# Optimization experiments

Hardware: AMD Instinct MI355X
Metric: run time of the kernel (lower is better)

## Reference

```python
import jax, jax.numpy as jnp
import numpy as np

DIM = 64
HEADS = 4
N_NODES = 50000
N_EDGES = 800000
NEG_SLOPE = 0.2


def setup_inputs() -> dict:
    key = jax.random.key(0)
    k1, k2, k3, k4, k5 = jax.random.split(key, 5)
    meta_x = jax.random.normal(k1, (N_NODES, DIM), dtype=jnp.float32)
    meta_edge_index = jax.random.randint(k2, (2, N_EDGES), 0, N_NODES, dtype=jnp.int64)
    # GATConv params: shared source/dest Linear (no bias), per-head attention vecs, output bias.
    glorot = float(np.sqrt(2.0 / (DIM + HEADS * DIM)))
    W = jax.random.normal(k3, (DIM, HEADS * DIM), dtype=jnp.float32) * glorot  # x @ W
    att_src = jax.random.normal(k4, (1, HEADS, DIM), dtype=jnp.float32) * glorot
    att_dst = jax.random.normal(k5, (1, HEADS, DIM), dtype=jnp.float32) * glorot
    bias = jnp.zeros((DIM,), dtype=jnp.float32)
    return {"meta_x": meta_x, "meta_edge_index": meta_edge_index,
            "W": W, "att_src": att_src, "att_dst": att_dst, "bias": bias}


def reference(meta_x, meta_edge_index, W, att_src, att_dst, bias):
    N = meta_x.shape[0]
    # PyG GATConv default: add self-loops
    loops = jnp.arange(N, dtype=meta_edge_index.dtype)
    edge = jnp.concatenate([meta_edge_index, jnp.stack([loops, loops])], axis=1)
    src, dst = edge[0], edge[1]

    x = (meta_x @ W).reshape(N, HEADS, DIM)            # [N, H, C]
    a_src = jnp.sum(x * att_src, axis=-1)              # [N, H]
    a_dst = jnp.sum(x * att_dst, axis=-1)              # [N, H]

    logits = a_src[src] + a_dst[dst]                   # [E, H]
    logits = jax.nn.leaky_relu(logits, NEG_SLOPE)

    # segment softmax over edges grouped by destination node
    seg_max = jax.ops.segment_max(logits, dst, num_segments=N)   # [N, H]
    ex = jnp.exp(logits - seg_max[dst])
    seg_sum = jax.ops.segment_sum(ex, dst, num_segments=N)
    alpha = ex / (seg_sum[dst] + 1e-16)                # [E, H]

    msg = x[src] * alpha[:, :, None]                   # [E, H, C]
    out = jax.ops.segment_sum(msg, dst, num_segments=N)  # [N, H, C]
    # concat=False -> mean over heads, then bias
    return out.mean(axis=1) + bias
```

## Files before the change

kernel.cpp:

```cpp
#include <hip/hip_runtime.h>
#include <hip/hip_bf16.h>
#include <math.h>

#define MAXDEG 64

__device__ __forceinline__ float lrelu(float v) { return v > 0.0f ? v : 0.2f * v; }

__global__ void prep_kernel(int4* __restrict__ cnt4, int n4, int N,
                            const float* __restrict__ W, const float* __restrict__ att_src,
                            const float* __restrict__ att_dst, float* __restrict__ wsrc,
                            float* __restrict__ wdst) {
  int idx = blockIdx.x * 256 + threadIdx.x;
  for (int i = idx; i < n4; i += gridDim.x * 256) {
    int base = i * 4;
    int4 v;
    v.x = (base < N) ? 1 : 0;
    v.y = (base + 1 < N) ? 1 : 0;
    v.z = (base + 2 < N) ? 1 : 0;
    v.w = (base + 3 < N) ? 1 : 0;
    cnt4[i] = v;
  }
  if (blockIdx.x == 0) {
    int t = threadIdx.x;
    int h = t >> 6, k = t & 63;
    const float* wrow = W + (size_t)k * 256 + h * 64;
    const float* as = att_src + h * 64;
    const float* ad = att_dst + h * 64;
    float ss = 0.f, sd = 0.f;
#pragma unroll
    for (int c = 0; c < 64; ++c) {
      float w = wrow[c];
      ss = fmaf(w, as[c], ss);
      sd = fmaf(w, ad[c], sd);
    }
    wsrc[k * 4 + h] = ss;
    wdst[k * 4 + h] = sd;
  }
}

__global__ void nh_kernel(const float* __restrict__ x, const float4* __restrict__ wsrc4,
                          const float4* __restrict__ wdst4, float4* __restrict__ asrc4,
                          float4* __restrict__ adst4, __hip_bfloat16* __restrict__ xh,
                          const int* __restrict__ ei, int* __restrict__ counts,
                          int E, int N, int nbh) {
  if (blockIdx.x < nbh) {
    int slice = blockIdx.x & 7;
    int bid = blockIdx.x >> 3;
    int nb = nbh >> 3;
    int chunk = (N + 7) >> 3;
    int lo = slice * chunk;
    int hi = lo + chunk; if (hi > N) hi = N;
    int E4 = E >> 2;
    const int4* d4p = (const int4*)(ei + E);
    int stride = nb * 256;
    for (int i = bid * 256 + threadIdx.x; i < E4; i += stride) {
      int4 d = d4p[i];
      if (d.x >= lo && d.x < hi) atomicAdd(&counts[d.x], 1);
      if (d.y >= lo && d.y < hi) atomicAdd(&counts[d.y], 1);
      if (d.z >= lo && d.z < hi) atomicAdd(&counts[d.z], 1);
      if (d.w >= lo && d.w < hi) atomicAdd(&counts[d.w], 1);
    }
    return;
  }
  int lane = threadIdx.x & 63;
  int n = (blockIdx.x - nbh) * 4 + (threadIdx.x >> 6);
  if (n >= N) return;
  float xv = x[(size_t)n * 64 + lane];
  xh[(size_t)n * 64 + lane] = __float2bfloat16(xv);
  float4 ws = wsrc4[lane], wd = wdst4[lane];
  float s0 = xv * ws.x, s1 = xv * ws.y, s2 = xv * ws.z, s3 = xv * ws.w;
  float d0 = xv * wd.x, d1 = xv * wd.y, d2 = xv * wd.z, d3 = xv * wd.w;
#pragma unroll
  for (int m = 1; m < 64; m <<= 1) {
    s0 += __shfl_xor(s0, m, 64); s1 += __shfl_xor(s1, m, 64);
    s2 += __shfl_xor(s2, m, 64); s3 += __shfl_xor(s3, m, 64);
    d0 += __shfl_xor(d0, m, 64); d1 += __shfl_xor(d1, m, 64);
    d2 += __shfl_xor(d2, m, 64); d3 += __shfl_xor(d3, m, 64);
  }
  if (lane == 0) {
    asrc4[n] = make_float4(s0, s1, s2, s3);
    adst4[n] = make_float4(d0, d1, d2, d3);
  }
}

__global__ void nattn_kernel(const float* __restrict__ x, const float4* __restrict__ wsrc4,
                             const float4* __restrict__ wdst4, float4* __restrict__ asrc4,
                             float4* __restrict__ adst4, __hip_bfloat16* __restrict__ xh,
                             int N) {
  int lane = threadIdx.x & 63;
  int n = blockIdx.x * 4 + (threadIdx.x >> 6);
  if (n >= N) return;
  float xv = x[(size_t)n * 64 + lane];
  xh[(size_t)n * 64 + lane] = __float2bfloat16(xv);
  float4 ws = wsrc4[lane], wd = wdst4[lane];
  float s0 = xv * ws.x, s1 = xv * ws.y, s2 = xv * ws.z, s3 = xv * ws.w;
  float d0 = xv * wd.x, d1 = xv * wd.y, d2 = xv * wd.z, d3 = xv * wd.w;
#pragma unroll
  for (int m = 1; m < 64; m <<= 1) {
    s0 += __shfl_xor(s0, m, 64); s1 += __shfl_xor(s1, m, 64);
    s2 += __shfl_xor(s2, m, 64); s3 += __shfl_xor(s3, m, 64);
    d0 += __shfl_xor(d0, m, 64); d1 += __shfl_xor(d1, m, 64);
    d2 += __shfl_xor(d2, m, 64); d3 += __shfl_xor(d3, m, 64);
  }
  if (lane == 0) {
    asrc4[n] = make_float4(s0, s1, s2, s3);
    adst4[n] = make_float4(d0, d1, d2, d3);
  }
}

__global__ void hist_kernel(const int* __restrict__ ei, int* __restrict__ counts, int E) {
  int e = blockIdx.x * 256 + threadIdx.x;
  if (e >= E) return;
  atomicAdd(&counts[ei[(size_t)E + e]], 1);
}

__global__ void scatter_kernel(const int* __restrict__ ei, int* __restrict__ cursor,
                               int* __restrict__ src_sorted, int E, int N) {
  int e = blockIdx.x * 256 + threadIdx.x;
  int ET = E + N;
  if (e >= ET) return;
  int src, dst;
  if (e < E) {
    src = ei[e];
    dst = ei[(size_t)E + e];
  } else {
    src = dst = e - E;
  }
  int pos = atomicAdd(&cursor[dst], 1);
  src_sorted[pos] = src;
}

__global__ void scatter8_kernel(const int* __restrict__ ei, int* __restrict__ cursor,
                                int* __restrict__ srt, int E, int N) {
  int slice = blockIdx.x & 7;
  int bid = blockIdx.x >> 3;
  int nb = gridDim.x >> 3;
  int chunk = (N + 7) >> 3;
  int lo = slice * chunk;
  int hi = lo + chunk; if (hi > N) hi = N;
  int E4 = E >> 2;
  const int4* s4p = (const int4*)ei;
  const int4* d4p = (const int4*)(ei + E);
  int stride = nb * 256;
  for (int i = bid * 256 + threadIdx.x; i < E4; i += stride) {
    int4 d4 = d4p[i];
    bool bx = (d4.x >= lo && d4.x < hi), by = (d4.y >= lo && d4.y < hi);
    bool bz = (d4.z >= lo && d4.z < hi), bw = (d4.w >= lo && d4.w < hi);
    if (!(bx || by || bz || bw)) continue;
    int4 s4 = s4p[i];
    if (bx) { int p = atomicAdd(&cursor[d4.x], 1); srt[p] = s4.x; }
    if (by) { int p = atomicAdd(&cursor[d4.y], 1); srt[p] = s4.y; }
    if (bz) { int p = atomicAdd(&cursor[d4.z], 1); srt[p] = s4.z; }
    if (bw) { int p = atomicAdd(&cursor[d4.w], 1); srt[p] = s4.w; }
  }
  for (int n = lo + bid * 256 + threadIdx.x; n < hi; n += stride) {
    int p = atomicAdd(&cursor[n], 1);
    srt[p] = n;
  }
}

__global__ void scanABC_kernel(const int* __restrict__ cnt, int* __restrict__ row,
                               int* __restrict__ cur, int N, int ntiles) {
  __shared__ int tl[256];
  __shared__ int part[256];
  int b = blockIdx.x, t = threadIdx.x;
  int s = 0;
  if (t < ntiles) {
    const int4* c4 = (const int4*)cnt + t * 64;
    for (int i = 0; i < 64; ++i) {
      int4 v = c4[i];
      s += v.x + v.y + v.z + v.w;
    }
  }
  tl[t] = s;
  __syncthreads();
  for (int d = 1; d < 256; d <<= 1) {
    int u = (t >= d) ? tl[t - d] : 0;
    __syncthreads();
    tl[t] += u;
    __syncthreads();
  }
  int tileoff = (b == 0) ? 0 : tl[b - 1];
  int idx = b * 256 + t;
  int c = (idx < N) ? cnt[idx] : 0;
  part[t] = c;
  __syncthreads();
  for (int d = 1; d < 256; d <<= 1) {
    int u = (t >= d) ? part[t - d] : 0;
    __syncthreads();
    part[t] += u;
    __syncthreads();
  }
  int exc = part[t] - c + tileoff;
  if (idx < N) {
    row[idx] = exc;
    cur[idx] = exc;
    if (idx == N - 1) row[N] = exc + c;
  }
}

__global__ void scanA_kernel(const int* __restrict__ cnt, int* __restrict__ tsum, int N) {
  int b = blockIdx.x, t = threadIdx.x;
  int idx = b * 256 + t;
  int v = (idx < N) ? cnt[idx] : 0;
#pragma unroll
  for (int m = 1; m < 64; m <<= 1) v += __shfl_xor(v, m, 64);
  __shared__ int ws[4];
  if ((t & 63) == 0) ws[t >> 6] = v;
  __syncthreads();
  if (t == 0) tsum[b] = ws[0] + ws[1] + ws[2] + ws[3];
}

__global__ void scanB_kernel(int* __restrict__ tsum, int ntiles) {
  __shared__ int part[256];
  int t = threadIdx.x;
  int carry = 0;
  for (int b0 = 0; b0 < ntiles; b0 += 256) {
    int idx = b0 + t;
    int v = (idx < ntiles) ? tsum[idx] : 0;
    part[t] = v;
    __syncthreads();
    for (int d = 1; d < 256; d <<= 1) {
      int u = (t >= d) ? part[t - d] : 0;
      __syncthreads();
      part[t] += u;
      __syncthreads();
    }
    if (idx < ntiles) tsum[idx] = part[t] - v + carry;
    carry += part[255];
    __syncthreads();
  }
}

__global__ void scanC_kernel(const int* __restrict__ cnt, const int* __restrict__ tsum,
                             int* __restrict__ row, int* __restrict__ cur, int N) {
  __shared__ int part[256];
  int b = blockIdx.x, t = threadIdx.x;
  int idx = b * 256 + t;
  int c = (idx < N) ? cnt[idx] : 0;
  part[t] = c;
  __syncthreads();
  for (int d = 1; d < 256; d <<= 1) {
    int u = (t >= d) ? part[t - d] : 0;
    __syncthreads();
    part[t] += u;
    __syncthreads();
  }
  int exc = part[t] - c + tsum[b];
  if (idx < N) {
    row[idx] = exc;
    cur[idx] = exc;
    if (idx == N - 1) row[N] = exc + c;
  }
}

__global__ __launch_bounds__(256) void agg_kernel(
    const int* __restrict__ srt, const int* __restrict__ row,
    const float4* __restrict__ asrc4, const float4* __restrict__ adst4,
    const __hip_bfloat16* __restrict__ xh, __hip_bfloat16* __restrict__ agg, int N) {
  __shared__ float4 alL[4][MAXDEG];
  __shared__ int slL[4][MAXDEG];
  int t = threadIdx.x, w = t >> 6, lane = t & 63;
  int n = blockIdx.x * 4 + w;
  if (n >= N) return;
  int start = row[n], end = row[n + 1];
  int deg = end - start;
  float4 ad = adst4[n];
  float t0 = 0.f, t1 = 0.f, t2 = 0.f, t3 = 0.f;
  if (deg <= MAXDEG) {
    for (int b = 0; b < deg; b += 64) {
      if (b + lane < deg) {
        int sl = srt[start + b + lane];
        float4 as = asrc4[sl];
        float4 e;
        e.x = __expf(lrelu(as.x + ad.x));
        e.y = __expf(lrelu(as.y + ad.y));
        e.z = __expf(lrelu(as.z + ad.z));
        e.w = __expf(lrelu(as.w + ad.w));
        alL[w][b + lane] = e;
        slL[w][b + lane] = sl;
        t0 += e.x; t1 += e.y; t2 += e.z; t3 += e.w;
      }
    }
  } else {
    for (int b = start; b < end; b += 64) {
      int idx = b + lane;
      if (idx < end) {
        int sl = srt[idx];
        float4 as = asrc4[sl];
        t0 += __expf(lrelu(as.x + ad.x));
        t1 += __expf(lrelu(as.y + ad.y));
        t2 += __expf(lrelu(as.z + ad.z));
        t3 += __expf(lrelu(as.w + ad.w));
      }
    }
  }
#pragma unroll
  for (int m = 1; m < 64; m <<= 1) {
    t0 += __shfl_xor(t0, m, 64);
    t1 += __shfl_xor(t1, m, 64);
    t2 += __shfl_xor(t2, m, 64);
    t3 += __shfl_xor(t3, m, 64);
  }
  float r0 = 0.25f / (t0 + 1e-16f), r1 = 0.25f / (t1 + 1e-16f);
  float r2 = 0.25f / (t2 + 1e-16f), r3 = 0.25f / (t3 + 1e-16f);
  float a0 = 0.f, a1 = 0.f, a2 = 0.f, a3 = 0.f;
  if (deg <= MAXDEG) {
    int j = 0;
    for (; j + 4 <= deg; j += 4) {
      float4 e0 = alL[w][j], e1 = alL[w][j + 1], e2 = alL[w][j + 2], e3 = alL[w][j + 3];
      int q0 = slL[w][j], q1 = slL[w][j + 1], q2 = slL[w][j + 2], q3 = slL[w][j + 3];
      float v0 = __bfloat162float(xh[(size_t)q0 * 64 + lane]);
      float v1 = __bfloat162float(xh[(size_t)q1 * 64 + lane]);
      float v2 = __bfloat162float(xh[(size_t)q2 * 64 + lane]);
      float v3 = __bfloat162float(xh[(size_t)q3 * 64 + lane]);
      a0 = fmaf(e0.x, v0, a0); a1 = fmaf(e0.y, v0, a1);
      a2 = fmaf(e0.z, v0, a2); a3 = fmaf(e0.w, v0, a3);
      a0 = fmaf(e1.x, v1, a0); a1 = fmaf(e1.y, v1, a1);
      a2 = fmaf(e1.z, v1, a2); a3 = fmaf(e1.w, v1, a3);
      a0 = fmaf(e2.x, v2, a0); a1 = fmaf(e2.y, v2, a1);
      a2 = fmaf(e2.z, v2, a2); a3 = fmaf(e2.w, v2, a3);
      a0 = fmaf(e3.x, v3, a0); a1 = fmaf(e3.y, v3, a1);
      a2 = fmaf(e3.z, v3, a2); a3 = fmaf(e3.w, v3, a3);
    }
    for (; j < deg; ++j) {
      float4 e0 = alL[w][j];
      int q0 = slL[w][j];
      float v0 = __bfloat162float(xh[(size_t)q0 * 64 + lane]);
      a0 = fmaf(e0.x, v0, a0); a1 = fmaf(e0.y, v0, a1);
      a2 = fmaf(e0.z, v0, a2); a3 = fmaf(e0.w, v0, a3);
    }
  } else {
    for (int b = start; b < end; b += 64) {
      int cnt = end - b;
      if (cnt > 64) cnt = 64;
      int idx = b + lane;
      int sl = 0;
      float e0 = 0.f, e1 = 0.f, e2 = 0.f, e3 = 0.f;
      if (idx < end) {
        sl = srt[idx];
        float4 as = asrc4[sl];
        e0 = __expf(lrelu(as.x + ad.x));
        e1 = __expf(lrelu(as.y + ad.y));
        e2 = __expf(lrelu(as.z + ad.z));
        e3 = __expf(lrelu(as.w + ad.w));
      }
      for (int j = 0; j < cnt; ++j) {
        int sj = __shfl(sl, j, 64);
        float b0 = __shfl(e0, j, 64), b1 = __shfl(e1, j, 64);
        float b2 = __shfl(e2, j, 64), b3 = __shfl(e3, j, 64);
        float v = __bfloat162float(xh[(size_t)sj * 64 + lane]);
        a0 = fmaf(b0, v, a0); a1 = fmaf(b1, v, a1);
        a2 = fmaf(b2, v, a2); a3 = fmaf(b3, v, a3);
      }
    }
  }
  __hip_bfloat16* ao = agg + (size_t)n * 256;
  ao[lane] = __float2bfloat16(a0 * r0);
  ao[64 + lane] = __float2bfloat16(a1 * r1);
  ao[128 + lane] = __float2bfloat16(a2 * r2);
  ao[192 + lane] = __float2bfloat16(a3 * r3);
}

__global__ __launch_bounds__(256) void proj_kernel(
    const __hip_bfloat16* __restrict__ agg, const float* __restrict__ W,
    const float* __restrict__ bias, float* __restrict__ out, int N) {
  __shared__ float aggL[4][256];
  __shared__ float pL[4][4][64];
  int t = threadIdx.x, w = t >> 6, lane = t & 63;
  float Wreg[64];
#pragma unroll
  for (int k = 0; k < 64; ++k) Wreg[k] = W[(size_t)k * 256 + w * 64 + lane];
  float bv = bias[lane];
  int ngroups = (N + 3) >> 2;
  for (int g = blockIdx.x; g < ngroups; g += gridDim.x) {
    int n0 = g * 4;
    __syncthreads();
    {
      int nn = n0 + w;
      if (nn < N) {
        ushort4 u = ((const ushort4*)(agg + (size_t)nn * 256))[t & 63];
        float4 f;
        f.x = __bfloat162float(*(__hip_bfloat16*)&u.x);
        f.y = __bfloat162float(*(__hip_bfloat16*)&u.y);
        f.z = __bfloat162float(*(__hip_bfloat16*)&u.z);
        f.w = __bfloat162float(*(__hip_bfloat16*)&u.w);
        *(float4*)&aggL[w][(t & 63) * 4] = f;
      } else {
        *(float4*)&aggL[w][(t & 63) * 4] = make_float4(0.f, 0.f, 0.f, 0.f);
      }
    }
    __syncthreads();
    float acc0 = 0.f, acc1 = 0.f, acc2 = 0.f, acc3 = 0.f;
#pragma unroll
    for (int k4 = 0; k4 < 16; ++k4) {
      float4 av0 = *(const float4*)&aggL[0][w * 64 + k4 * 4];
      float4 av1 = *(const float4*)&aggL[1][w * 64 + k4 * 4];
      float4 av2 = *(const float4*)&aggL[2][w * 64 + k4 * 4];
      float4 av3 = *(const float4*)&aggL[3][w * 64 + k4 * 4];
      float w0 = Wreg[k4 * 4 + 0], w1 = Wreg[k4 * 4 + 1];
      float w2 = Wreg[k4 * 4 + 2], w3 = Wreg[k4 * 4 + 3];
      acc0 = fmaf(av0.x, w0, acc0); acc0 = fmaf(av0.y, w1, acc0);
      acc0 = fmaf(av0.z, w2, acc0); acc0 = fmaf(av0.w, w3, acc0);
      acc1 = fmaf(av1.x, w0, acc1); acc1 = fmaf(av1.y, w1, acc1);
      acc1 = fmaf(av1.z, w2, acc1); acc1 = fmaf(av1.w, w3, acc1);
      acc2 = fmaf(av2.x, w0, acc2); acc2 = fmaf(av2.y, w1, acc2);
      acc2 = fmaf(av2.z, w2, acc2); acc2 = fmaf(av2.w, w3, acc2);
      acc3 = fmaf(av3.x, w0, acc3); acc3 = fmaf(av3.y, w1, acc3);
      acc3 = fmaf(av3.z, w2, acc3); acc3 = fmaf(av3.w, w3, acc3);
    }
    pL[w][0][lane] = acc0;
    pL[w][1][lane] = acc1;
    pL[w][2][lane] = acc2;
    pL[w][3][lane] = acc3;
    __syncthreads();
    int nn = n0 + w;
    if (nn < N) {
      out[(size_t)nn * 64 + lane] = pL[0][w][lane] + pL[1][w][lane] +
                                    pL[2][w][lane] + pL[3][w][lane] + bv;
    }
  }
}

extern "C" void kernel_launch(void* const* d_in, const int* in_sizes, int n_in,
                              void* d_out, int out_size, void* d_ws, size_t ws_size,
                              hipStream_t stream) {
  const float* meta_x = (const float*)d_in[0];
  const int* ei = (const int*)d_in[1];
  const float* W = (const float*)d_in[2];
  const float* att_src = (const float*)d_in[3];
  const float* att_dst = (const float*)d_in[4];
  const float* bias = (const float*)d_in[5];
  float* out = (float*)d_out;

  int N = in_sizes[0] / 64;
  int E = in_sizes[1] / 2;
  int ET = E + N;
  int ntiles = (N + 255) / 256;

  char* ws = (char*)d_ws;
  size_t off = 0;
  auto alloc = [&](size_t bytes) {
    size_t o = off;
    off += (bytes + 255) & ~(size_t)255;
    return o;
  };
  size_t o_wsrc = alloc(64 * 4 * sizeof(float));
  size_t o_wdst = alloc(64 * 4 * sizeof(float));
  size_t o_asrc = alloc((size_t)N * 4 * sizeof(float));
  size_t o_adst = alloc((size_t)N * 4 * sizeof(float));
  size_t o_cnt = alloc((size_t)ntiles * 256 * sizeof(int));
  size_t o_row = alloc(((size_t)N + 1) * sizeof(int));
  size_t o_cur = alloc((size_t)N * sizeof(int));
  size_t o_srt = alloc((size_t)ET * sizeof(int));
  size_t o_ts = alloc((size_t)ntiles * sizeof(int));
  size_t o_xh = alloc((size_t)N * 64 * sizeof(__hip_bfloat16));
  size_t o_agg = alloc((size_t)N * 256 * sizeof(__hip_bfloat16));
  (void)ws_size;

  float* wsrc = (float*)(ws + o_wsrc);
  float* wdst = (float*)(ws + o_wdst);
  float4* asrc4 = (float4*)(ws + o_asrc);
  float4* adst4 = (float4*)(ws + o_adst);
  int* cnt = (int*)(ws + o_cnt);
  int* row = (int*)(ws + o_row);
  int* cur = (int*)(ws + o_cur);
  int* srt = (int*)(ws + o_srt);
  int* tsum = (int*)(ws + o_ts);
  __hip_bfloat16* xh = (__hip_bfloat16*)(ws + o_xh);
  __hip_bfloat16* aggp = (__hip_bfloat16*)(ws + o_agg);

  int n4 = ntiles * 64;
  prep_kernel<<<64, 256, 0, stream>>>((int4*)cnt, n4, N, W, att_src, att_dst, wsrc, wdst);

  if ((E & 3) == 0) {
    int nbh = 2048;
    int nbn = (N + 3) / 4;
    nh_kernel<<<nbh + nbn, 256, 0, stream>>>(meta_x, (const float4*)wsrc,
                                             (const float4*)wdst, asrc4, adst4, xh,
                                             ei, cnt, E, N, nbh);
  } else {
    nattn_kernel<<<(N + 3) / 4, 256, 0, stream>>>(meta_x, (const float4*)wsrc,
                                                  (const float4*)wdst, asrc4, adst4, xh, N);
    hist_kernel<<<(E + 255) / 256, 256, 0, stream>>>(ei, cnt, E);
  }

  if (ntiles <= 256) {
    scanABC_kernel<<<ntiles, 256, 0, stream>>>(cnt, row, cur, N, ntiles);
  } else {
    scanA_kernel<<<ntiles, 256, 0, stream>>>(cnt, tsum, N);
    scanB_kernel<<<1, 256, 0, stream>>>(tsum, ntiles);
    scanC_kernel<<<ntiles, 256, 0, stream>>>(cnt, tsum, row, cur, N);
  }

  if ((E & 3) == 0) {
    scatter8_kernel<<<2048, 256, 0, stream>>>(ei, cur, srt, E, N);
  } else {
    scatter_kernel<<<(ET + 255) / 256, 256, 0, stream>>>(ei, cur, srt, E, N);
  }

  agg_kernel<<<(N + 3) / 4, 256, 0, stream>>>(srt, row, asrc4, adst4, xh, aggp, N);
  int ngroups = (N + 3) / 4;
  int pgrid = ngroups < 1024 ? ngroups : 1024;
  proj_kernel<<<pgrid, 256, 0, stream>>>(aggp, W, bias, out, N);
}
```

Before: 188.5 us.

## Replace global-atomic degree histogram with LDS-privatized partial histograms plus merge

Degree counting moves out of the fused node/histogram kernel into a new kernel. Each of 256 blocks builds a shared-memory histogram for one of 8 node slices over 1/32 of the edges, and a merge kernel sums the 32 partials per bin and adds the self-loop count. This replaces contended global atomics with LDS atomics. In exchange it adds two launches, a partial-count buffer in workspace, and extra global traffic to write and read the partials.

```diff
diff --git a/kernel.cpp b/kernel.cpp
--- a/kernel.cpp
+++ b/kernel.cpp
@@ -3,6 +3,7 @@
 #include <math.h>
 
 #define MAXDEG 64
+#define MAXCHUNK 6400
 
 __device__ __forceinline__ float lrelu(float v) { return v > 0.0f ? v : 0.2f * v; }
 
@@ -38,48 +39,44 @@
   }
 }
 
-__global__ void nh_kernel(const float* __restrict__ x, const float4* __restrict__ wsrc4,
-                          const float4* __restrict__ wdst4, float4* __restrict__ asrc4,
-                          float4* __restrict__ adst4, __hip_bfloat16* __restrict__ xh,
-                          const int* __restrict__ ei, int* __restrict__ counts,
-                          int E, int N, int nbh) {
-  if (blockIdx.x < nbh) {
-    int slice = blockIdx.x & 7;
-    int bid = blockIdx.x >> 3;
-    int nb = nbh >> 3;
-    int chunk = (N + 7) >> 3;
-    int lo = slice * chunk;
-    int hi = lo + chunk; if (hi > N) hi = N;
-    int E4 = E >> 2;
-    const int4* d4p = (const int4*)(ei + E);
-    int stride = nb * 256;
-    for (int i = bid * 256 + threadIdx.x; i < E4; i += stride) {
-      int4 d = d4p[i];
-      if (d.x >= lo && d.x < hi) atomicAdd(&counts[d.x], 1);
-      if (d.y >= lo && d.y < hi) atomicAdd(&counts[d.y], 1);
-      if (d.z >= lo && d.z < hi) atomicAdd(&counts[d.z], 1);
-      if (d.w >= lo && d.w < hi) atomicAdd(&counts[d.w], 1);
-    }
-    return;
-  }
-  int lane = threadIdx.x & 63;
-  int n = (blockIdx.x - nbh) * 4 + (threadIdx.x >> 6);
-  if (n >= N) return;
-  float xv = x[(size_t)n * 64 + lane];
-  xh[(size_t)n * 64 + lane] = __float2bfloat16(xv);
-  float4 ws = wsrc4[lane], wd = wdst4[lane];
-  float s0 = xv * ws.x, s1 = xv * ws.y, s2 = xv * ws.z, s3 = xv * ws.w;
-  float d0 = xv * wd.x, d1 = xv * wd.y, d2 = xv * wd.z, d3 = xv * wd.w;
-#pragma unroll
-  for (int m = 1; m < 64; m <<= 1) {
-    s0 += __shfl_xor(s0, m, 64); s1 += __shfl_xor(s1, m, 64);
-    s2 += __shfl_xor(s2, m, 64); s3 += __shfl_xor(s3, m, 64);
-    d0 += __shfl_xor(d0, m, 64); d1 += __shfl_xor(d1, m, 64);
-    d2 += __shfl_xor(d2, m, 64); d3 += __shfl_xor(d3, m, 64);
-  }
-  if (lane == 0) {
-    asrc4[n] = make_float4(s0, s1, s2, s3);
-    adst4[n] = make_float4(d0, d1, d2, d3);
+__global__ __launch_bounds__(256) void histpart_kernel(
+    const int* __restrict__ ei, int* __restrict__ cntpart, int E, int N, int chunkN) {
+  __shared__ int h[MAXCHUNK];
+  int s = blockIdx.x >> 5, p = blockIdx.x & 31;
+  int lo = s * chunkN;
+  int hi = lo + chunkN; if (hi > N) hi = N;
+  for (int i = threadIdx.x; i < chunkN; i += 256) h[i] = 0;
+  __syncthreads();
+  int E4 = E >> 2;
+  int c0 = (int)(((long long)p * E4) >> 5);
+  int c1 = (int)(((long long)(p + 1) * E4) >> 5);
+  const int4* d4p = (const int4*)(ei + E);
+  for (int i = c0 + threadIdx.x; i < c1; i += 256) {
+    int4 d = d4p[i];
+    if (d.x >= lo && d.x < hi) atomicAdd(&h[d.x - lo], 1);
+    if (d.y >= lo && d.y < hi) atomicAdd(&h[d.y - lo], 1);
+    if (d.z >= lo && d.z < hi) atomicAdd(&h[d.z - lo], 1);
+    if (d.w >= lo && d.w < hi) atomicAdd(&h[d.w - lo], 1);
+  }
+  __syncthreads();
+  int* out = cntpart + (size_t)blockIdx.x * chunkN;
+  for (int i = threadIdx.x; i < chunkN; i += 256) out[i] = h[i];
+}
+
+__global__ void merge_kernel(const int* __restrict__ cntpart, int* __restrict__ cnt,
+                             int N, int chunkN, int nbins) {
+  int bin = blockIdx.x * 256 + threadIdx.x;
+  if (bin >= nbins) return;
+  if (bin < N) {
+    int s = bin / chunkN;
+    int i = bin - s * chunkN;
+    const int* base = cntpart + (size_t)(s * 32) * chunkN + i;
+    int sum = 1;
+#pragma unroll
+    for (int p = 0; p < 32; ++p) sum += base[(size_t)p * chunkN];
+    cnt[bin] = sum;
+  } else {
+    cnt[bin] = 0;
   }
 }
 
@@ -437,6 +434,7 @@
   int E = in_sizes[1] / 2;
   int ET = E + N;
   int ntiles = (N + 255) / 256;
+  int chunkN = (N + 7) / 8;
 
   char* ws = (char*)d_ws;
   size_t off = 0;
@@ -454,6 +452,7 @@
   size_t o_cur = alloc((size_t)N * sizeof(int));
   size_t o_srt = alloc((size_t)ET * sizeof(int));
   size_t o_ts = alloc((size_t)ntiles * sizeof(int));
+  size_t o_cp = alloc((size_t)256 * chunkN * sizeof(int));
   size_t o_xh = alloc((size_t)N * 64 * sizeof(__hip_bfloat16));
   size_t o_agg = alloc((size_t)N * 256 * sizeof(__hip_bfloat16));
   (void)ws_size;
@@ -467,18 +466,19 @@
   int* cur = (int*)(ws + o_cur);
   int* srt = (int*)(ws + o_srt);
   int* tsum = (int*)(ws + o_ts);
+  int* cntpart = (int*)(ws + o_cp);
   __hip_bfloat16* xh = (__hip_bfloat16*)(ws + o_xh);
   __hip_bfloat16* aggp = (__hip_bfloat16*)(ws + o_agg);
 
   int n4 = ntiles * 64;
   prep_kernel<<<64, 256, 0, stream>>>((int4*)cnt, n4, N, W, att_src, att_dst, wsrc, wdst);
 
-  if ((E & 3) == 0) {
-    int nbh = 2048;
-    int nbn = (N + 3) / 4;
-    nh_kernel<<<nbh + nbn, 256, 0, stream>>>(meta_x, (const float4*)wsrc,
-                                             (const float4*)wdst, asrc4, adst4, xh,
-                                             ei, cnt, E, N, nbh);
+  bool ldsHist = ((E & 3) == 0) && (chunkN <= MAXCHUNK);
+  if (ldsHist) {
+    histpart_kernel<<<256, 256, 0, stream>>>(ei, cntpart, E, N, chunkN);
+    nattn_kernel<<<(N + 3) / 4, 256, 0, stream>>>(meta_x, (const float4*)wsrc,
+                                                  (const float4*)wdst, asrc4, adst4, xh, N);
+    merge_kernel<<<ntiles, 256, 0, stream>>>(cntpart, cnt, N, chunkN, ntiles * 256);
   } else {
     nattn_kernel<<<(N + 3) / 4, 256, 0, stream>>>(meta_x, (const float4*)wsrc,
                                                   (const float4*)wdst, asrc4, adst4, xh, N);
```

New measurement: 168.4 us (median of 2 runs). -10.7%, faster.
